# Optimization experiments

Measured on AMD Instinct MI355X. Metric: run time of the kernel, lower is better.

Reference implementation:

```python
import jax, jax.numpy as jnp
import numpy as np

# (in_dim, out_dim) for fc1..fc14, hard-coded in the torch module
DIMS = [(12,12),(12,11),(11,10),(10,9),(9,8),(8,7),(7,6),(6,7),(7,8),(8,9),(9,10),(10,11),(11,12),(12,2)]
BATCH = 2_000_000


def setup_inputs() -> dict:
    key = jax.random.key(0)
    keys = jax.random.split(key, 2 * len(DIMS) + 1)
    inp = {"x": jax.random.normal(keys[0], (BATCH, 12), dtype=jnp.float32)}
    for i, (din, dout) in enumerate(DIMS):
        s = 1.0 / np.sqrt(din)  # torch nn.Linear default init range
        inp[f"w{i+1}"] = jax.random.uniform(keys[2*i+1], (dout, din), jnp.float32, -s, s)
        inp[f"b{i+1}"] = jax.random.uniform(keys[2*i+2], (dout,), jnp.float32, -s, s)
    return inp


def _forward(x, Ws, Bs):
    lin = lambda h, i: h @ Ws[i].T + Bs[i]
    # encoder half: fc1..fc6 with ReLU, saving identities 1..6
    ids = []
    h = x
    for i in range(6):
        h = jax.nn.relu(lin(h, i))
        ids.append(h)
    # bottleneck fc7
    h = jax.nn.relu(lin(h, 6))
    # decoder half: fc8..fc13, each adds the matching identity before ReLU
    # fc8 (+id6), fc9 (+id5), ..., fc13 (+id1)
    for i in range(7, 13):
        h = jax.nn.relu(lin(h, i) + ids[12 - i])
    # fc14 + softmax over class dim
    return jax.nn.softmax(lin(h, 13), axis=1)


def reference(x, w1, b1, w2, b2, w3, b3, w4, b4, w5, b5, w6, b6, w7, b7,
              w8, b8, w9, b9, w10, b10, w11, b11, w12, b12, w13, b13, w14, b14):
    Ws = [w1, w2, w3, w4, w5, w6, w7, w8, w9, w10, w11, w12, w13, w14]
    Bs = [b1, b2, b3, b4, b5, b6, b7, b8, b9, b10, b11, b12, b13, b14]
    return _forward(x, Ws, Bs)
```

## Files before the change

kernel.cpp:

```cpp
#include <hip/hip_runtime.h>
#include <math.h>

#define DEV __device__ __forceinline__


typedef _Float16 h2 __attribute__((ext_vector_type(2)));

DEV unsigned h2u(h2 h) { union { h2 h; unsigned u; } c; c.h = h; return c.u; }
DEV h2 u2h(unsigned u) { union { unsigned u; h2 h; } c; c.u = u; return c.h; }

#define UW1  0
#define UW2  72
#define UW3  140
#define UW4  200
#define UW5  248
#define UW6  288
#define UW7  316
#define UW8  340
#define UW9  364
#define UW10 396
#define UW11 432
#define UW12 484
#define UW13 540
#define UW14 612
#define OB1  624
#define OB2  636
#define OB3  648
#define OB4  660
#define OB5  672
#define OB6  680
#define OB7  688
#define OB8  696
#define OB9  704
#define OB10 712
#define OB11 724
#define OB12 736
#define OB13 748
#define OB14 760
#define WTOT 764

__device__ __attribute__((aligned(16))) unsigned Wq[WTOT];

__global__ void repack_kernel(
    const float* w1,  const float* b1,  const float* w2,  const float* b2,
    const float* w3,  const float* b3,  const float* w4,  const float* b4,
    const float* w5,  const float* b5,  const float* w6,  const float* b6,
    const float* w7,  const float* b7,  const float* w8,  const float* b8,
    const float* w9,  const float* b9,  const float* w10, const float* b10,
    const float* w11, const float* b11, const float* w12, const float* b12,
    const float* w13, const float* b13, const float* w14, const float* b14) {
    struct L { const float* w; const float* b; int din, dout, uw, ob; };
    const L ls[14] = {
        {w1,  b1,  12, 12, UW1,  OB1},  {w2,  b2,  12, 11, UW2,  OB2},
        {w3,  b3,  11, 10, UW3,  OB3},  {w4,  b4,  10,  9, UW4,  OB4},
        {w5,  b5,   9,  8, UW5,  OB5},  {w6,  b6,   8,  7, UW6,  OB6},
        {w7,  b7,   7,  6, UW7,  OB7},  {w8,  b8,   6,  7, UW8,  OB8},
        {w9,  b9,   7,  8, UW9,  OB9},  {w10, b10,  8,  9, UW10, OB10},
        {w11, b11,  9, 10, UW11, OB11}, {w12, b12, 10, 11, UW12, OB12},
        {w13, b13, 11, 12, UW13, OB13}, {w14, b14, 12,  2, UW14, OB14}};
    const int tid = threadIdx.x;
    for (int s = 0; s < 14; ++s) {
        const L& l = ls[s];
        const int kp = (l.din + 1) / 2;
        for (int i = tid; i < l.dout * kp; i += 256) {
            int o = i / kp, p = i % kp;
            float a = l.w[o * l.din + 2 * p];
            float c = (2 * p + 1 < l.din) ? l.w[o * l.din + 2 * p + 1] : 0.0f;
            h2 h; h.x = (_Float16)a; h.y = (_Float16)c;
            Wq[l.uw + i] = h2u(h);
        }
        for (int i = tid; i < l.dout; i += 256)
            Wq[l.ob + i] = __float_as_uint(l.b[i]);
    }
}

template <int DIN, int DOUT, int UW, int OB>
DEV void lind(const h2* a, float* acc) {
    constexpr int KP = (DIN + 1) / 2;
    const unsigned* __restrict__ wq =
        (const unsigned*)__builtin_assume_aligned(&Wq[UW], 16);
#pragma unroll
    for (int ot = 0; ot < DOUT; ot += 4) {
        const int oe = (ot + 4 < DOUT) ? (ot + 4) : DOUT;
        unsigned wt[24];
#pragma unroll
        for (int i = 0; i < 24; ++i)
            if (i < (oe - ot) * KP) wt[i] = wq[ot * KP + i];
#pragma unroll
        for (int o = ot; o < oe; ++o) acc[o] = __uint_as_float(Wq[OB + o]);
#pragma unroll
        for (int p = 0; p < KP; ++p) {
            h2 ak = a[p];
#pragma unroll
            for (int o = ot; o < oe; ++o)
                acc[o] = __builtin_amdgcn_fdot2(
                    ak, u2h(wt[(o - ot) * KP + p]), acc[o], false);
        }
    }
}

template <int DIN, int DOUT, int UW, int OB>
DEV void lind_skip(const h2* a, const float* skip, float* acc) {
    constexpr int KP = (DIN + 1) / 2;
    const unsigned* __restrict__ wq =
        (const unsigned*)__builtin_assume_aligned(&Wq[UW], 16);
#pragma unroll
    for (int ot = 0; ot < DOUT; ot += 4) {
        const int oe = (ot + 4 < DOUT) ? (ot + 4) : DOUT;
        unsigned wt[24];
#pragma unroll
        for (int i = 0; i < 24; ++i)
            if (i < (oe - ot) * KP) wt[i] = wq[ot * KP + i];
#pragma unroll
        for (int o = ot; o < oe; ++o)
            acc[o] = __uint_as_float(Wq[OB + o]) + skip[o];
#pragma unroll
        for (int p = 0; p < KP; ++p) {
            h2 ak = a[p];
#pragma unroll
            for (int o = ot; o < oe; ++o)
                acc[o] = __builtin_amdgcn_fdot2(
                    ak, u2h(wt[(o - ot) * KP + p]), acc[o], false);
        }
    }
}

template <int N>
DEV void relu_keep_pack(const float* acc, float* idf, h2* p) {
#pragma unroll
    for (int i = 0; i < N; ++i) idf[i] = fmaxf(acc[i], 0.0f);
#pragma unroll
    for (int i = 0; i < (N + 1) / 2; ++i) {
        h2 h;
        h.x = (_Float16)idf[2 * i];
        h.y = (_Float16)((2 * i + 1 < N) ? idf[2 * i + 1] : 0.0f);
        p[i] = h;
    }
}

template <int N>
DEV void relu_pack(const float* acc, h2* p) {
#pragma unroll
    for (int i = 0; i < (N + 1) / 2; ++i) {
        float a0 = fmaxf(acc[2 * i], 0.0f);
        float a1 = (2 * i + 1 < N) ? fmaxf(acc[2 * i + 1], 0.0f) : 0.0f;
        h2 h; h.x = (_Float16)a0; h.y = (_Float16)a1;
        p[i] = h;
    }
}

__global__ void __launch_bounds__(256, 4)
csnet14_kernel(const float* __restrict__ x, float* __restrict__ out, int n) {
    int t = blockIdx.x * blockDim.x + threadIdx.x;
    if (t >= n) return;

    const float4* xr = reinterpret_cast<const float4*>(x + (size_t)t * 12);
    float4 v0 = xr[0], v1 = xr[1], v2 = xr[2];
    float xin[12] = {v0.x, v0.y, v0.z, v0.w, v1.x, v1.y, v1.z, v1.w,
                     v2.x, v2.y, v2.z, v2.w};
    h2 xp[6];
#pragma unroll
    for (int i = 0; i < 6; ++i) {
        h2 h; h.x = (_Float16)xin[2 * i]; h.y = (_Float16)xin[2 * i + 1];
        xp[i] = h;
    }

    float a1[12]; lind<12, 12, UW1, OB1>(xp, a1);
    float id1[12]; h2 c1[6]; relu_keep_pack<12>(a1, id1, c1);
    float a2[11]; lind<12, 11, UW2, OB2>(c1, a2);
    float id2[11]; h2 c2[6]; relu_keep_pack<11>(a2, id2, c2);
    float a3[10]; lind<11, 10, UW3, OB3>(c2, a3);
    float id3[10]; h2 c3[5]; relu_keep_pack<10>(a3, id3, c3);
    float a4[9];  lind<10,  9, UW4, OB4>(c3, a4);
    float id4[9];  h2 c4[5]; relu_keep_pack<9>(a4, id4, c4);
    float a5[8];  lind< 9,  8, UW5, OB5>(c4, a5);
    float id5[8];  h2 c5[4]; relu_keep_pack<8>(a5, id5, c5);
    float a6[7];  lind< 8,  7, UW6, OB6>(c5, a6);
    float id6[7];  h2 c6[4]; relu_keep_pack<7>(a6, id6, c6);

    float a7[6];  lind< 7,  6, UW7, OB7>(c6, a7);
    h2 q7[3];  relu_pack<6>(a7, q7);

    float a8[7];  lind_skip< 6,  7, UW8,  OB8 >(q7,  id6, a8);
    h2 q8[4];  relu_pack<7>(a8, q8);
    float a9[8];  lind_skip< 7,  8, UW9,  OB9 >(q8,  id5, a9);
    h2 q9[4];  relu_pack<8>(a9, q9);
    float a10[9]; lind_skip< 8,  9, UW10, OB10>(q9,  id4, a10);
    h2 q10[5]; relu_pack<9>(a10, q10);
    float a11[10]; lind_skip< 9, 10, UW11, OB11>(q10, id3, a11);
    h2 q11[5]; relu_pack<10>(a11, q11);
    float a12[11]; lind_skip<10, 11, UW12, OB12>(q11, id2, a12);
    h2 q12[6]; relu_pack<11>(a12, q12);
    float a13[12]; lind_skip<11, 12, UW13, OB13>(q12, id1, a13);
    h2 q13[6]; relu_pack<12>(a13, q13);

    float l[2];   lind<12,  2, UW14, OB14>(q13, l);
    float m  = fmaxf(l[0], l[1]);
    float e0 = __expf(l[0] - m);
    float e1 = __expf(l[1] - m);
    float inv = __builtin_amdgcn_rcpf(e0 + e1);

    float2 o;
    o.x = e0 * inv;
    o.y = e1 * inv;
    reinterpret_cast<float2*>(out)[t] = o;
}

extern "C" void kernel_launch(void* const* d_in, const int* in_sizes, int n_in,
                              void* d_out, int out_size, void* d_ws, size_t ws_size,
                              hipStream_t stream) {
    const float* x   = (const float*)d_in[0];
    const float* w1  = (const float*)d_in[1];  const float* b1  = (const float*)d_in[2];
    const float* w2  = (const float*)d_in[3];  const float* b2  = (const float*)d_in[4];
    const float* w3  = (const float*)d_in[5];  const float* b3  = (const float*)d_in[6];
    const float* w4  = (const float*)d_in[7];  const float* b4  = (const float*)d_in[8];
    const float* w5  = (const float*)d_in[9];  const float* b5  = (const float*)d_in[10];
    const float* w6  = (const float*)d_in[11]; const float* b6  = (const float*)d_in[12];
    const float* w7  = (const float*)d_in[13]; const float* b7  = (const float*)d_in[14];
    const float* w8  = (const float*)d_in[15]; const float* b8  = (const float*)d_in[16];
    const float* w9  = (const float*)d_in[17]; const float* b9  = (const float*)d_in[18];
    const float* w10 = (const float*)d_in[19]; const float* b10 = (const float*)d_in[20];
    const float* w11 = (const float*)d_in[21]; const float* b11 = (const float*)d_in[22];
    const float* w12 = (const float*)d_in[23]; const float* b12 = (const float*)d_in[24];
    const float* w13 = (const float*)d_in[25]; const float* b13 = (const float*)d_in[26];
    const float* w14 = (const float*)d_in[27]; const float* b14 = (const float*)d_in[28];
    float* out = (float*)d_out;

    const int n = in_sizes[0] / 12;

    repack_kernel<<<1, 256, 0, stream>>>(
        w1, b1, w2, b2, w3, b3, w4, b4, w5, b5, w6, b6, w7, b7,
        w8, b8, w9, b9, w10, b10, w11, b11, w12, b12, w13, b13, w14, b14);

    dim3 block(256);
    dim3 grid((n + 255) / 256);
    csnet14_kernel<<<grid, block, 0, stream>>>(x, out, n);
}
```

Measured before the change: 233.1 us.

## Spill encoder skip activations to LDS as packed fp16 and parallelize repack

Stores the six encoder identity activations as packed fp16 pairs in shared memory instead of keeping them as fp32 registers. The decoder adds each skip in packed half precision after the fp16 conversion and applies ReLU with a packed max. The goal is lower register pressure and higher occupancy, so the __launch_bounds__ minimum-blocks hint is dropped. The repack kernel now runs one block per layer with 64 threads instead of a single looping block. The costs are 30 KB of LDS per block, extra LDS traffic, and a different rounding order (skip added in fp16 rather than fp32), which changes numerics slightly.

```diff
diff --git a/kernel.cpp b/kernel.cpp
--- a/kernel.cpp
+++ b/kernel.cpp
@@ -58,20 +58,18 @@
         {w9,  b9,   7,  8, UW9,  OB9},  {w10, b10,  8,  9, UW10, OB10},
         {w11, b11,  9, 10, UW11, OB11}, {w12, b12, 10, 11, UW12, OB12},
         {w13, b13, 11, 12, UW13, OB13}, {w14, b14, 12,  2, UW14, OB14}};
+    const L& l = ls[blockIdx.x];
     const int tid = threadIdx.x;
-    for (int s = 0; s < 14; ++s) {
-        const L& l = ls[s];
-        const int kp = (l.din + 1) / 2;
-        for (int i = tid; i < l.dout * kp; i += 256) {
-            int o = i / kp, p = i % kp;
-            float a = l.w[o * l.din + 2 * p];
-            float c = (2 * p + 1 < l.din) ? l.w[o * l.din + 2 * p + 1] : 0.0f;
-            h2 h; h.x = (_Float16)a; h.y = (_Float16)c;
-            Wq[l.uw + i] = h2u(h);
-        }
-        for (int i = tid; i < l.dout; i += 256)
-            Wq[l.ob + i] = __float_as_uint(l.b[i]);
-    }
+    const int kp = (l.din + 1) / 2;
+    for (int i = tid; i < l.dout * kp; i += blockDim.x) {
+        int o = i / kp, p = i % kp;
+        float a = l.w[o * l.din + 2 * p];
+        float c = (2 * p + 1 < l.din) ? l.w[o * l.din + 2 * p + 1] : 0.0f;
+        h2 h; h.x = (_Float16)a; h.y = (_Float16)c;
+        Wq[l.uw + i] = h2u(h);
+    }
+    for (int i = tid; i < l.dout; i += blockDim.x)
+        Wq[l.ob + i] = __float_as_uint(l.b[i]);
 }
 
 template <int DIN, int DOUT, int UW, int OB>
@@ -99,59 +97,23 @@
     }
 }
 
-template <int DIN, int DOUT, int UW, int OB>
-DEV void lind_skip(const h2* a, const float* skip, float* acc) {
-    constexpr int KP = (DIN + 1) / 2;
-    const unsigned* __restrict__ wq =
-        (const unsigned*)__builtin_assume_aligned(&Wq[UW], 16);
-#pragma unroll
-    for (int ot = 0; ot < DOUT; ot += 4) {
-        const int oe = (ot + 4 < DOUT) ? (ot + 4) : DOUT;
-        unsigned wt[24];
-#pragma unroll
-        for (int i = 0; i < 24; ++i)
-            if (i < (oe - ot) * KP) wt[i] = wq[ot * KP + i];
-#pragma unroll
-        for (int o = ot; o < oe; ++o)
-            acc[o] = __uint_as_float(Wq[OB + o]) + skip[o];
-#pragma unroll
-        for (int p = 0; p < KP; ++p) {
-            h2 ak = a[p];
-#pragma unroll
-            for (int o = ot; o < oe; ++o)
-                acc[o] = __builtin_amdgcn_fdot2(
-                    ak, u2h(wt[(o - ot) * KP + p]), acc[o], false);
-        }
-    }
-}
-
 template <int N>
-DEV void relu_keep_pack(const float* acc, float* idf, h2* p) {
-#pragma unroll
-    for (int i = 0; i < N; ++i) idf[i] = fmaxf(acc[i], 0.0f);
+DEV void relu_pack(const float* acc, h2* p) {
 #pragma unroll
     for (int i = 0; i < (N + 1) / 2; ++i) {
         h2 h;
-        h.x = (_Float16)idf[2 * i];
-        h.y = (_Float16)((2 * i + 1 < N) ? idf[2 * i + 1] : 0.0f);
-        p[i] = h;
-    }
-}
-
-template <int N>
-DEV void relu_pack(const float* acc, h2* p) {
-#pragma unroll
-    for (int i = 0; i < (N + 1) / 2; ++i) {
-        float a0 = fmaxf(acc[2 * i], 0.0f);
-        float a1 = (2 * i + 1 < N) ? fmaxf(acc[2 * i + 1], 0.0f) : 0.0f;
-        h2 h; h.x = (_Float16)a0; h.y = (_Float16)a1;
-        p[i] = h;
-    }
-}
-
-__global__ void __launch_bounds__(256, 4)
+        h.x = (_Float16)acc[2 * i];
+        h.y = (_Float16)((2 * i + 1 < N) ? acc[2 * i + 1] : 0.0f);
+        h2 z; z.x = (_Float16)0.0f; z.y = (_Float16)0.0f;
+        p[i] = __builtin_elementwise_max(h, z);
+    }
+}
+
+__global__ void __launch_bounds__(256)
 csnet14_kernel(const float* __restrict__ x, float* __restrict__ out, int n) {
-    int t = blockIdx.x * blockDim.x + threadIdx.x;
+    __shared__ unsigned lds[30 * 256];
+    const int tid = threadIdx.x;
+    int t = blockIdx.x * blockDim.x + tid;
     if (t >= n) return;
 
     const float4* xr = reinterpret_cast<const float4*>(x + (size_t)t * 12);
@@ -166,33 +128,80 @@
     }
 
     float a1[12]; lind<12, 12, UW1, OB1>(xp, a1);
-    float id1[12]; h2 c1[6]; relu_keep_pack<12>(a1, id1, c1);
+    h2 c1[6]; relu_pack<12>(a1, c1);
+#pragma unroll
+    for (int i = 0; i < 6; ++i) lds[(0 + i) * 256 + tid] = h2u(c1[i]);
     float a2[11]; lind<12, 11, UW2, OB2>(c1, a2);
-    float id2[11]; h2 c2[6]; relu_keep_pack<11>(a2, id2, c2);
+    h2 c2[6]; relu_pack<11>(a2, c2);
+#pragma unroll
+    for (int i = 0; i < 6; ++i) lds[(6 + i) * 256 + tid] = h2u(c2[i]);
     float a3[10]; lind<11, 10, UW3, OB3>(c2, a3);
-    float id3[10]; h2 c3[5]; relu_keep_pack<10>(a3, id3, c3);
+    h2 c3[5]; relu_pack<10>(a3, c3);
+#pragma unroll
+    for (int i = 0; i < 5; ++i) lds[(12 + i) * 256 + tid] = h2u(c3[i]);
     float a4[9];  lind<10,  9, UW4, OB4>(c3, a4);
-    float id4[9];  h2 c4[5]; relu_keep_pack<9>(a4, id4, c4);
+    h2 c4[5]; relu_pack<9>(a4, c4);
+#pragma unroll
+    for (int i = 0; i < 5; ++i) lds[(17 + i) * 256 + tid] = h2u(c4[i]);
     float a5[8];  lind< 9,  8, UW5, OB5>(c4, a5);
-    float id5[8];  h2 c5[4]; relu_keep_pack<8>(a5, id5, c5);
+    h2 c5[4]; relu_pack<8>(a5, c5);
+#pragma unroll
+    for (int i = 0; i < 4; ++i) lds[(22 + i) * 256 + tid] = h2u(c5[i]);
     float a6[7];  lind< 8,  7, UW6, OB6>(c5, a6);
-    float id6[7];  h2 c6[4]; relu_keep_pack<7>(a6, id6, c6);
+    h2 c6[4]; relu_pack<7>(a6, c6);
+#pragma unroll
+    for (int i = 0; i < 4; ++i) lds[(26 + i) * 256 + tid] = h2u(c6[i]);
 
     float a7[6];  lind< 7,  6, UW7, OB7>(c6, a7);
-    h2 q7[3];  relu_pack<6>(a7, q7);
-
-    float a8[7];  lind_skip< 6,  7, UW8,  OB8 >(q7,  id6, a8);
-    h2 q8[4];  relu_pack<7>(a8, q8);
-    float a9[8];  lind_skip< 7,  8, UW9,  OB9 >(q8,  id5, a9);
-    h2 q9[4];  relu_pack<8>(a9, q9);
-    float a10[9]; lind_skip< 8,  9, UW10, OB10>(q9,  id4, a10);
-    h2 q10[5]; relu_pack<9>(a10, q10);
-    float a11[10]; lind_skip< 9, 10, UW11, OB11>(q10, id3, a11);
-    h2 q11[5]; relu_pack<10>(a11, q11);
-    float a12[11]; lind_skip<10, 11, UW12, OB12>(q11, id2, a12);
-    h2 q12[6]; relu_pack<11>(a12, q12);
-    float a13[12]; lind_skip<11, 12, UW13, OB13>(q12, id1, a13);
-    h2 q13[6]; relu_pack<12>(a13, q13);
+    h2 q7[3]; relu_pack<6>(a7, q7);
+
+    h2 z; z.x = (_Float16)0.0f; z.y = (_Float16)0.0f;
+
+    float a8[7];  lind< 6,  7, UW8,  OB8 >(q7, a8);
+    h2 q8[4];
+#pragma unroll
+    for (int i = 0; i < 4; ++i) {
+        h2 h; h.x = (_Float16)a8[2 * i];
+        h.y = (_Float16)((2 * i + 1 < 7) ? a8[2 * i + 1] : 0.0f);
+        q8[i] = __builtin_elementwise_max(h + u2h(lds[(26 + i) * 256 + tid]), z);
+    }
+    float a9[8];  lind< 7,  8, UW9,  OB9 >(q8, a9);
+    h2 q9[4];
+#pragma unroll
+    for (int i = 0; i < 4; ++i) {
+        h2 h; h.x = (_Float16)a9[2 * i]; h.y = (_Float16)a9[2 * i + 1];
+        q9[i] = __builtin_elementwise_max(h + u2h(lds[(22 + i) * 256 + tid]), z);
+    }
+    float a10[9]; lind< 8,  9, UW10, OB10>(q9, a10);
+    h2 q10[5];
+#pragma unroll
+    for (int i = 0; i < 5; ++i) {
+        h2 h; h.x = (_Float16)a10[2 * i];
+        h.y = (_Float16)((2 * i + 1 < 9) ? a10[2 * i + 1] : 0.0f);
+        q10[i] = __builtin_elementwise_max(h + u2h(lds[(17 + i) * 256 + tid]), z);
+    }
+    float a11[10]; lind< 9, 10, UW11, OB11>(q10, a11);
+    h2 q11[5];
+#pragma unroll
+    for (int i = 0; i < 5; ++i) {
+        h2 h; h.x = (_Float16)a11[2 * i]; h.y = (_Float16)a11[2 * i + 1];
+        q11[i] = __builtin_elementwise_max(h + u2h(lds[(12 + i) * 256 + tid]), z);
+    }
+    float a12[11]; lind<10, 11, UW12, OB12>(q11, a12);
+    h2 q12[6];
+#pragma unroll
+    for (int i = 0; i < 6; ++i) {
+        h2 h; h.x = (_Float16)a12[2 * i];
+        h.y = (_Float16)((2 * i + 1 < 11) ? a12[2 * i + 1] : 0.0f);
+        q12[i] = __builtin_elementwise_max(h + u2h(lds[(6 + i) * 256 + tid]), z);
+    }
+    float a13[12]; lind<11, 12, UW13, OB13>(q12, a13);
+    h2 q13[6];
+#pragma unroll
+    for (int i = 0; i < 6; ++i) {
+        h2 h; h.x = (_Float16)a13[2 * i]; h.y = (_Float16)a13[2 * i + 1];
+        q13[i] = __builtin_elementwise_max(h + u2h(lds[(0 + i) * 256 + tid]), z);
+    }
 
     float l[2];   lind<12,  2, UW14, OB14>(q13, l);
     float m  = fmaxf(l[0], l[1]);
@@ -228,7 +237,7 @@
 
     const int n = in_sizes[0] / 12;
 
-    repack_kernel<<<1, 256, 0, stream>>>(
+    repack_kernel<<<14, 64, 0, stream>>>(
         w1, b1, w2, b2, w3, b3, w4, b4, w5, b5, w6, b6, w7, b7,
         w8, b8, w9, b9, w10, b10, w11, b11, w12, b12, w13, b13, w14, b14);
 
```

Result: no change. 229.6 us (-1.5%).
